# Performance work log

Hardware: AMD Instinct MI355X
Metric: run time of the kernel (lower is better)

The kernel has to match this reference:

```python
import jax, jax.numpy as jnp
import numpy as np
from jax import lax

DN = ('NCHW', 'OIHW', 'NCHW')


def conv3x3(x, w, groups=1):
    return lax.conv_general_dilated(x, w, window_strides=(1, 1),
                                    padding=((1, 1), (1, 1)),
                                    dimension_numbers=DN,
                                    feature_group_count=groups)


def conv1x1(x, w):
    return lax.conv_general_dilated(x, w, window_strides=(1, 1),
                                    padding=((0, 0), (0, 0)),
                                    dimension_numbers=DN)


def l2_normalize(t, eps=1e-12):
    n = jnp.sqrt(jnp.sum(t * t, axis=-1, keepdims=True))
    return t / jnp.maximum(n, eps)


def setup_inputs() -> dict:
    key = jax.random.key(0)
    ks = jax.random.split(key, 10)
    B, C, H, W = 4, 64, 256, 256
    heads = 8
    s = 0.05
    return {
        'x': jax.random.normal(ks[0], (B, C, H, W), jnp.float32),
        'w_iem': jax.random.normal(ks[1], (C, C, 3, 3), jnp.float32) * s,
        'w_nem': jax.random.normal(ks[2], (C, C, 3, 3), jnp.float32) * s,
        'w_iem_dw': jax.random.normal(ks[3], (C, 1, 3, 3), jnp.float32) * s,
        'w_nem_dw': jax.random.normal(ks[4], (C, 1, 3, 3), jnp.float32) * s,
        'w_q': jax.random.normal(ks[5], (C, C, 1, 1), jnp.float32) * s,
        'w_k': jax.random.normal(ks[6], (C, C, 1, 1), jnp.float32) * s,
        'w_v': jax.random.normal(ks[7], (C, C, 1, 1), jnp.float32) * s,
        'w_proj': jax.random.normal(ks[8], (C, C, 1, 1), jnp.float32) * s,
        'temperature': jnp.ones((1, heads, 1, 1, 1, 1), jnp.float32),
    }


def igam_forward(x, w_iem, w_nem, w_iem_dw, w_nem_dw, w_q, w_k, w_v, w_proj,
                 temperature, num_heads=8, window_size=8):
    b, c, h, w = x.shape
    ws = window_size
    pad_h = (ws - h % ws) % ws
    pad_w = (ws - w % ws) % ws
    if pad_h or pad_w:  # replicate pad on right/bottom (static)
        x = jnp.pad(x, ((0, 0), (0, 0), (0, pad_h), (0, pad_w)), mode='edge')
    hp, wp = x.shape[-2:]
    heads = num_heads
    d = c // heads
    nh, nw = hp // ws, wp // ws

    illumination_map = conv3x3(jax.nn.sigmoid(conv3x3(x, w_iem)), w_iem_dw, groups=c)
    noise_map = conv3x3(jax.nn.sigmoid(conv3x3(x, w_nem)), w_nem_dw, groups=c)
    illum_scalar = jnp.mean(illumination_map, axis=1, keepdims=True)  # (b,1,hp,wp)
    noise_scalar = jnp.mean(noise_map, axis=1, keepdims=True)

    q = conv1x1(illumination_map, w_q)
    k = conv1x1(noise_map, w_k)
    v = conv1x1(x, w_v)

    def to_windows(t):  # (b,c,hp,wp) -> (b,heads,nh,nw,ws*ws,d)
        t = t.reshape(b, heads, d, hp, wp).transpose(0, 1, 3, 4, 2)
        t = t.reshape(b, heads, nh, ws, nw, ws, d).transpose(0, 1, 2, 4, 3, 5, 6)
        return t.reshape(b, heads, nh, nw, ws * ws, d)

    def scalar_to_windows(t):  # (b,1,hp,wp) -> (b,1,nh,nw,ws*ws,1)
        t = t.reshape(b, 1, nh, ws, nw, ws).transpose(0, 1, 2, 4, 3, 5)
        return t.reshape(b, 1, nh, nw, ws * ws, 1)

    qw = l2_normalize(to_windows(q)) * (1.0 + scalar_to_windows(illum_scalar))
    kw = l2_normalize(to_windows(k)) * jnp.clip(1.0 - scalar_to_windows(noise_scalar), 0.0, 1.0)
    vw = to_windows(v)

    scale = d ** (-0.5)
    attn = jnp.einsum('bhnmqd,bhnmkd->bhnmqk', qw, kw) * scale * temperature
    attn = jax.nn.softmax(attn, axis=-1)
    outw = jnp.einsum('bhnmqk,bhnmkd->bhnmqd', attn, vw)

    # merge windows back to (b, c, hp, wp)
    outw = outw.reshape(b, heads, nh, nw, ws, ws, d).transpose(0, 1, 6, 2, 4, 3, 5)
    out = outw.reshape(b, heads * d, nh * ws, nw * ws)
    if pad_h or pad_w:
        out = out[:, :, :h, :w]
    return conv1x1(out, w_proj)


def reference(x, w_iem, w_nem, w_iem_dw, w_nem_dw, w_q, w_k, w_v, w_proj,
              temperature):
    return igam_forward(x, w_iem, w_nem, w_iem_dw, w_nem_dw, w_q, w_k, w_v,
                        w_proj, temperature)
```

## Files before the change

### kernel.cpp

```cpp
#include <hip/hip_runtime.h>
#include <math.h>

#define W_ 256
#define H_ 256
#define HW 65536
#define CC 64

typedef _Float16 h16;
typedef _Float16 half8 __attribute__((ext_vector_type(8)));
typedef float f32x4  __attribute__((ext_vector_type(4)));
typedef float f32x16 __attribute__((ext_vector_type(16)));

__device__ __forceinline__ unsigned pk2(float a, float b) {
  union { h16 h[2]; unsigned u; } c;
  c.h[0] = (h16)a; c.h[1] = (h16)b;
  return c.u;
}
__device__ __forceinline__ void plswap(unsigned &a, unsigned &b) {
  asm volatile("v_permlane32_swap_b32 %0, %1" : "+v"(a), "+v"(b));
}

__global__ __launch_bounds__(256) void k_wprep(
    const float* __restrict__ wi, const float* __restrict__ wn, h16* __restrict__ Bt)
{
  int i = blockIdx.x * 256 + threadIdx.x;
  if (i >= 128 * 576) return;
  int co = i / 576, k = i - co * 576;
  int tap = k >> 6, ci = k & 63;
  const float* src = (co < 64) ? wi : wn;
  int c = co & 63;
  Bt[i] = (h16)src[(c * 64 + ci) * 9 + tap];
}

__global__ __launch_bounds__(256) void k_wprep2(
    const float* __restrict__ wq, const float* __restrict__ wk,
    const float* __restrict__ wv, const float* __restrict__ wp,
    const float* __restrict__ wdw1, const float* __restrict__ wdw2,
    h16* __restrict__ W)
{
  int i = blockIdx.x * 256 + threadIdx.x;
  if (i >= 17536) return;
  if (i < 16384) {
    int m = i >> 12, e = i & 4095;
    const float* s = (m == 0) ? wq : (m == 1) ? wk : (m == 2) ? wv : wp;
    W[i] = (h16)s[e];
  } else {
    int e = i - 16384;
    int pass = e / 576, rem = e - pass * 576;
    int tap = rem >> 6, c = rem & 63;
    const float* s = pass ? wdw2 : wdw1;
    W[i] = (h16)s[c * 9 + tap];
  }
}

__global__ __launch_bounds__(256) void k_xpose(
    const float* __restrict__ x, h16* __restrict__ xT)
{
  __shared__ __align__(16) char sm[64 * 132];
  const int tid = threadIdx.x;
  const int xt = blockIdx.x, y = blockIdx.y, b = blockIdx.z;
  const int x0 = xt * 64;
  const float* xb = x + ((size_t)b * CC) * HW + y * W_ + x0;
  const int ci = tid >> 2, q = tid & 3;
#pragma unroll
  for (int k = 0; k < 4; ++k) {
    const int pc = q + k * 4;
    float4 v = *(const float4*)(xb + (size_t)ci * HW + pc * 4);
    const int px = pc * 4;
    *(h16*)(sm + (px + 0) * 132 + ci * 2) = (h16)v.x;
    *(h16*)(sm + (px + 1) * 132 + ci * 2) = (h16)v.y;
    *(h16*)(sm + (px + 2) * 132 + ci * 2) = (h16)v.z;
    *(h16*)(sm + (px + 3) * 132 + ci * 2) = (h16)v.w;
  }
  __syncthreads();
  h16* dst = xT + (((size_t)b * 256 + y) * 256 + x0) * 64;
#pragma unroll
  for (int it = 0; it < 2; ++it) {
    int task = tid + it * 256;
    int px = task >> 3, c8 = task & 7;
    int4 d = *(const int4*)(sm + px * 132 + c8 * 16);
    *(int4*)(dst + px * 64 + c8 * 8) = d;
  }
}

__global__ __launch_bounds__(512) void k_conv3x3x2(
    const h16* __restrict__ xT, const h16* __restrict__ Bt,
    h16* __restrict__ T1, h16* __restrict__ T2)
{
  __shared__ __align__(16) char lds[38016];

  const int tid = threadIdx.x;
  const int b = blockIdx.z, ry = blockIdx.y, cx = blockIdx.x;
  const int y0 = ry * 2, x0 = cx * 64;

  {
    const h16* xb = xT + ((size_t)b * 256) * 256 * 64;
    int4 zero4; zero4.x = zero4.y = zero4.z = zero4.w = 0;
#pragma unroll
    for (int it = 0; it < 5; ++it) {
      int idx = tid + it * 512;
      if (idx < 2112) {
        int pxr = idx >> 3, c8 = idx & 7;
        int r = pxr / 66, c = pxr - r * 66;
        int gy = y0 - 1 + r, gx = x0 - 1 + c;
        int4 d = zero4;
        if ((unsigned)gy < 256u && (unsigned)gx < 256u)
          d = *(const int4*)(xb + ((size_t)(gy * 256 + gx)) * 64 + c8 * 8);
        *(int4*)(lds + pxr * 144 + c8 * 16) = d;
      }
    }
  }
  __syncthreads();

  const int wv = tid >> 6, lane = tid & 63;
  const int wn_ = wv & 3;
  const int wm_ = wv >> 2;
  const int cob = wn_ * 32;
  const int pxb = wm_ * 64;
  const int lg = lane >> 4, lr = lane & 15;

  const char* pB[4];
#pragma unroll
  for (int pi = 0; pi < 4; ++pi) {
    int opx = (pxb + pi * 16 + lr) & 63;
    pB[pi] = lds + (wm_ * 66 + opx) * 144 + lg * 16;
  }
  const h16* wb0 = Bt + (size_t)(cob + lr) * 576 + lg * 8;
  const h16* wb1 = wb0 + 16 * 576;

  f32x4 acc[2][4];
#pragma unroll
  for (int i = 0; i < 2; ++i)
#pragma unroll
    for (int j = 0; j < 4; ++j) acc[i][j] = (f32x4){0.f, 0.f, 0.f, 0.f};

#pragma unroll
  for (int tap = 0; tap < 9; ++tap) {
    const int dy = tap / 3, dx = tap - dy * 3;
#pragma unroll
    for (int kh = 0; kh < 2; ++kh) {
      const int loff = (dy * 66 + dx) * 144 + kh * 64;
      const int koff = tap * 64 + kh * 32;
      half8 a0 = *(const half8*)(wb0 + koff);
      half8 a1 = *(const half8*)(wb1 + koff);
      half8 b0 = *(const half8*)(pB[0] + loff);
      half8 b1 = *(const half8*)(pB[1] + loff);
      half8 b2 = *(const half8*)(pB[2] + loff);
      half8 b3 = *(const half8*)(pB[3] + loff);
      acc[0][0] = __builtin_amdgcn_mfma_f32_16x16x32_f16(a0, b0, acc[0][0], 0, 0, 0);
      acc[0][1] = __builtin_amdgcn_mfma_f32_16x16x32_f16(a0, b1, acc[0][1], 0, 0, 0);
      acc[0][2] = __builtin_amdgcn_mfma_f32_16x16x32_f16(a0, b2, acc[0][2], 0, 0, 0);
      acc[0][3] = __builtin_amdgcn_mfma_f32_16x16x32_f16(a0, b3, acc[0][3], 0, 0, 0);
      acc[1][0] = __builtin_amdgcn_mfma_f32_16x16x32_f16(a1, b0, acc[1][0], 0, 0, 0);
      acc[1][1] = __builtin_amdgcn_mfma_f32_16x16x32_f16(a1, b1, acc[1][1], 0, 0, 0);
      acc[1][2] = __builtin_amdgcn_mfma_f32_16x16x32_f16(a1, b2, acc[1][2], 0, 0, 0);
      acc[1][3] = __builtin_amdgcn_mfma_f32_16x16x32_f16(a1, b3, acc[1][3], 0, 0, 0);
    }
  }
  __syncthreads();

#pragma unroll
  for (int ni = 0; ni < 2; ++ni) {
#pragma unroll
    for (int pi = 0; pi < 4; ++pi) {
      const int opx = (pxb + pi * 16 + lr) & 63;
      const int pxid = wm_ * 64 + opx;
      const int co = cob + ni * 16 + lg * 4;
      float s0 = 1.f / (1.f + __expf(-acc[ni][pi][0]));
      float s1 = 1.f / (1.f + __expf(-acc[ni][pi][1]));
      float s2 = 1.f / (1.f + __expf(-acc[ni][pi][2]));
      float s3 = 1.f / (1.f + __expf(-acc[ni][pi][3]));
      uint2 d; d.x = pk2(s0, s1); d.y = pk2(s2, s3);
      *(uint2*)(lds + pxid * 272 + co * 2) = d;
    }
  }
  __syncthreads();

  {
    int px = tid >> 3, chg = tid & 7;
#pragma unroll
    for (int seg = 0; seg < 4; ++seg) {
      int t = seg >> 1, rr = seg & 1;
      int4 d = *(const int4*)(lds + (rr * 64 + px) * 272 + t * 128 + chg * 16);
      h16* dst = (t ? T2 : T1) + (((size_t)b * 256 + (y0 + rr)) * 256 + (x0 + px)) * 64 + chg * 8;
      *(int4*)dst = d;
    }
  }
}

#define HALO 0
#define INC  0
#define DWW  14400
#define SIN  16704
#define INA  17216
#define INB  26432

__global__ __launch_bounds__(512, 8) void k_megaattn(
    const h16* __restrict__ T1g, const h16* __restrict__ T2g,
    const h16* __restrict__ xT, const h16* __restrict__ Wall,
    const float* __restrict__ temp, float* __restrict__ out)
{
  __shared__ __align__(16) char sm[35648];
  const int tid = threadIdx.x;
  const int wv = tid >> 6, lane = tid & 63;
  const int lg = lane >> 4, lr = lane & 15;
  const int wn = wv & 3;
  const int wm = wv >> 2;

  const int u = blockIdx.x;
  const int xcd = u & 7, idx = u >> 3;
  const int flat = xcd * 512 + idx;
  const int b = flat >> 10, rem = flat & 1023;
  const int wy = rem >> 5, wx = rem & 31;
  const int y0 = wy * 8, x0 = wx * 8;

  half8 wf[4][2];
#pragma unroll
  for (int m = 0; m < 4; ++m)
#pragma unroll
    for (int ks = 0; ks < 2; ++ks)
      wf[m][ks] = *(const half8*)(Wall + m * 4096 + (wn * 16 + lr) * 64 + ks * 32 + lg * 8);
  const float thv = temp[wn * 2 + (lg >> 1)];

  int4 zero4; zero4.x = zero4.y = zero4.z = zero4.w = 0;
  int4 h1r[2], h2r[2], xtr;
#pragma unroll
  for (int i = 0; i < 2; ++i) {
    int cc = tid + i * 512;
    bool act = cc < 800;
    int prow = act ? (cc >> 3) : 0;
    int c8 = cc & 7;
    int hy = prow / 10, hx = prow - hy * 10;
    int gy = y0 - 1 + hy, gx = x0 - 1 + hx;
    bool ok = act && (unsigned)gy < 256u && (unsigned)gx < 256u;
    size_t ga = (((size_t)b * 256 + gy) * 256 + gx) * (size_t)64 + c8 * 8;
    h1r[i] = ok ? *(const int4*)(T1g + ga) : zero4;
    h2r[i] = ok ? *(const int4*)(T2g + ga) : zero4;
  }
  const size_t wbase = (((size_t)b * 256 + y0) * 256 + x0) * 64;
  xtr = *(const int4*)(xT + wbase + (size_t)(tid >> 6) * 16384 + (tid & 63) * 8);

#pragma unroll
  for (int i = 0; i < 2; ++i) {
    int cc = tid + i * 512;
    if (cc < 800) *(int4*)(sm + HALO + (cc >> 3) * 144 + (cc & 7) * 16) = h1r[i];
  }
  if (tid < 144) {
    int4 d = *(const int4*)(Wall + 16384 + tid * 8);
    *(int4*)(sm + DWW + tid * 16) = d;
  }
  __syncthreads();

  const half8 hz8 = {(h16)0, (h16)0, (h16)0, (h16)0, (h16)0, (h16)0, (h16)0, (h16)0};
#pragma unroll
  for (int pass = 0; pass < 2; ++pass) {
    const int outb = pass ? INB : INA;
    {
      const int px = tid >> 3, c8 = tid & 7;
      const int py = px >> 3, pxx = px & 7;
      half8 af = hz8;
#pragma unroll
      for (int tap = 0; tap < 9; ++tap) {
        const int dy = tap / 3, dx = tap - dy * 3;
        half8 v  = *(const half8*)(sm + HALO + ((py + dy) * 10 + pxx + dx) * 144 + c8 * 16);
        half8 w8 = *(const half8*)(sm + DWW + pass * 1152 + tap * 128 + c8 * 16);
        af += v * w8;
      }
      *(half8*)(sm + outb + px * 144 + c8 * 16) = af;
    }
    __syncthreads();
    if (pass == 0) {
#pragma unroll
      for (int i = 0; i < 2; ++i) {
        int cc = tid + i * 512;
        if (cc < 800) *(int4*)(sm + HALO + (cc >> 3) * 144 + (cc & 7) * 16) = h2r[i];
      }
      __syncthreads();
    }
  }

  {
    int py = tid >> 6, off = tid & 63;
    int px = py * 8 + (off >> 3);
    *(int4*)(sm + INC + px * 144 + (off & 7) * 16) = xtr;
  }
  if (tid < 128) {
    int which = tid >> 6, px = tid & 63;
    const char* row = sm + (which ? INB : INA) + px * 144;
    float s = 0.f;
#pragma unroll
    for (int j = 0; j < 8; ++j) {
      half8 v = *(const half8*)(row + j * 16);
#pragma unroll
      for (int e = 0; e < 8; ++e) s += (float)v[e];
    }
    *(float*)(sm + SIN + which * 256 + px * 4) = s * (1.f / 64.f);
  }
  __syncthreads();

  f32x4 aq[2], ak[2], av[2];
#pragma unroll
  for (int pi = 0; pi < 2; ++pi) {
    aq[pi] = (f32x4){0.f, 0.f, 0.f, 0.f};
    ak[pi] = (f32x4){0.f, 0.f, 0.f, 0.f};
    av[pi] = (f32x4){0.f, 0.f, 0.f, 0.f};
  }
#pragma unroll
  for (int pi = 0; pi < 2; ++pi)
#pragma unroll
    for (int ks = 0; ks < 2; ++ks) {
      const int boff = (wm * 32 + pi * 16 + lr) * 144 + ks * 64 + lg * 16;
      half8 b0 = *(const half8*)(sm + INA + boff);
      half8 b1 = *(const half8*)(sm + INB + boff);
      half8 b2 = *(const half8*)(sm + INC + boff);
      aq[pi] = __builtin_amdgcn_mfma_f32_16x16x32_f16(wf[0][ks], b0, aq[pi], 0, 0, 0);
      ak[pi] = __builtin_amdgcn_mfma_f32_16x16x32_f16(wf[1][ks], b1, ak[pi], 0, 0, 0);
      av[pi] = __builtin_amdgcn_mfma_f32_16x16x32_f16(wf[2][ks], b2, av[pi], 0, 0, 0);
    }
  __syncthreads();

#pragma unroll
  for (int pi = 0; pi < 2; ++pi) {
    const int px = wm * 32 + pi * 16 + lr;
    const float si = *(const float*)(sm + SIN + px * 4);
    const float sn = *(const float*)(sm + SIN + 256 + px * 4);
    float s2 = aq[pi][0]*aq[pi][0] + aq[pi][1]*aq[pi][1] + aq[pi][2]*aq[pi][2] + aq[pi][3]*aq[pi][3];
    float qs = (1.f + si) * 0.35355339059327373f * thv /
               fmaxf(sqrtf(s2 + __shfl_xor(s2, 16)), 1e-12f);
    float k2 = ak[pi][0]*ak[pi][0] + ak[pi][1]*ak[pi][1] + ak[pi][2]*ak[pi][2] + ak[pi][3]*ak[pi][3];
    float ks2 = fminf(fmaxf(1.f - sn, 0.f), 1.f) /
                fmaxf(sqrtf(k2 + __shfl_xor(k2, 16)), 1e-12f);
    uint2 dq; dq.x = pk2(aq[pi][0]*qs, aq[pi][1]*qs); dq.y = pk2(aq[pi][2]*qs, aq[pi][3]*qs);
    uint2 dk; dk.x = pk2(ak[pi][0]*ks2, ak[pi][1]*ks2); dk.y = pk2(ak[pi][2]*ks2, ak[pi][3]*ks2);
    *(uint2*)(sm + INA + px * 144 + (wn * 16 + lg * 4) * 2) = dq;
    *(uint2*)(sm + INB + px * 144 + (wn * 16 + lg * 4) * 2) = dk;
#pragma unroll
    for (int r = 0; r < 4; ++r)
      *(h16*)(sm + INC + (wn * 16 + lg * 4 + r) * 144 + px * 2) = (h16)av[pi][r];
  }
  __syncthreads();

  const int l31 = lane & 31, hi = lane >> 5;
  const half8 hz = hz8;
  const f32x16 z16 = {0.f,0.f,0.f,0.f,0.f,0.f,0.f,0.f,0.f,0.f,0.f,0.f,0.f,0.f,0.f,0.f};
  {
    const int h = wv;
    half8 kfr[2], qfr[2];
#pragma unroll
    for (int kt = 0; kt < 2; ++kt)
      kfr[kt] = hi ? hz : *(const half8*)(sm + INB + (kt * 32 + l31) * 144 + h * 16);
#pragma unroll
    for (int qt = 0; qt < 2; ++qt)
      qfr[qt] = hi ? hz : *(const half8*)(sm + INA + (qt * 32 + l31) * 144 + h * 16);

#pragma unroll
    for (int qt = 0; qt < 2; ++qt) {
      f32x16 s0 = __builtin_amdgcn_mfma_f32_32x32x16_f16(kfr[0], qfr[qt], z16, 0, 0, 0);
      f32x16 s1 = __builtin_amdgcn_mfma_f32_32x32x16_f16(kfr[1], qfr[qt], z16, 0, 0, 0);
      float mx = s0[0];
#pragma unroll
      for (int i = 1; i < 16; ++i) mx = fmaxf(mx, s0[i]);
#pragma unroll
      for (int i = 0; i < 16; ++i) mx = fmaxf(mx, s1[i]);
      mx = fmaxf(mx, __shfl_xor(mx, 32));
      float sum = 0.f;
#pragma unroll
      for (int i = 0; i < 16; ++i) { s0[i] = __expf(s0[i] - mx); sum += s0[i]; }
#pragma unroll
      for (int i = 0; i < 16; ++i) { s1[i] = __expf(s1[i] - mx); sum += s1[i]; }
      sum += __shfl_xor(sum, 32);
      const float inv = 1.f / sum;
#pragma unroll
      for (int i = 0; i < 16; ++i) { s0[i] *= inv; s1[i] *= inv; }

      half8 pa[4];
#pragma unroll
      for (int st = 0; st < 4; ++st) {
        const int rb = (st & 1) * 8;
        float p0, p1, p2, p3, p4, p5, p6, p7;
        if (st < 2) {
          p0 = s0[rb+0]; p1 = s0[rb+1]; p2 = s0[rb+2]; p3 = s0[rb+3];
          p4 = s0[rb+4]; p5 = s0[rb+5]; p6 = s0[rb+6]; p7 = s0[rb+7];
        } else {
          p0 = s1[rb+0]; p1 = s1[rb+1]; p2 = s1[rb+2]; p3 = s1[rb+3];
          p4 = s1[rb+4]; p5 = s1[rb+5]; p6 = s1[rb+6]; p7 = s1[rb+7];
        }
        unsigned x0_ = pk2(p0, p1), x1_ = pk2(p2, p3);
        unsigned y0_ = pk2(p4, p5), y1_ = pk2(p6, p7);
        plswap(x0_, y0_);
        plswap(x1_, y1_);
        union { unsigned uu4[4]; half8 h; } uu;
        uu.uu4[0] = x0_; uu.uu4[1] = x1_; uu.uu4[2] = y0_; uu.uu4[3] = y1_;
        pa[st] = uu.h;
      }
      f32x16 oacc = z16;
#pragma unroll
      for (int st = 0; st < 4; ++st) {
        half8 vfr = (l31 < 8)
          ? *(const half8*)(sm + INC + (h * 8 + l31) * 144 + (st * 16 + hi * 8) * 2)
          : hz;
        oacc = __builtin_amdgcn_mfma_f32_32x32x16_f16(pa[st], vfr, oacc, 0, 0, 0);
      }
      if (l31 < 8) {
#pragma unroll
        for (int r = 0; r < 16; ++r) {
          const int q = qt * 32 + (r & 3) + 8 * (r >> 2) + 4 * hi;
          *(h16*)(sm + INA + q * 144 + (h * 8 + l31) * 2) = (h16)oacc[r];
        }
      }
    }
  }
  __syncthreads();

  f32x4 pacc[2];
#pragma unroll
  for (int pi = 0; pi < 2; ++pi) pacc[pi] = (f32x4){0.f, 0.f, 0.f, 0.f};
#pragma unroll
  for (int pi = 0; pi < 2; ++pi)
#pragma unroll
    for (int ks = 0; ks < 2; ++ks) {
      half8 bfr = *(const half8*)(sm + INA + (wm * 32 + pi * 16 + lr) * 144 + ks * 64 + lg * 16);
      pacc[pi] = __builtin_amdgcn_mfma_f32_16x16x32_f16(wf[3][ks], bfr, pacc[pi], 0, 0, 0);
    }
#pragma unroll
  for (int pi = 0; pi < 2; ++pi) {
    const int px = wm * 32 + pi * 16 + lr;
    const int py = px >> 3, pxx = px & 7;
    const int co = wn * 16 + lg * 4;
    float* ob = out + ((size_t)(b * CC + co)) * HW + (size_t)(y0 + py) * W_ + (x0 + pxx);
    ob[0]      = pacc[pi][0];
    ob[HW]     = pacc[pi][1];
    ob[2 * HW] = pacc[pi][2];
    ob[3 * HW] = pacc[pi][3];
  }
}

extern "C" void kernel_launch(void* const* d_in, const int* in_sizes, int n_in,
                              void* d_out, int out_size, void* d_ws, size_t ws_size,
                              hipStream_t stream) {
  const float* x        = (const float*)d_in[0];
  const float* w_iem    = (const float*)d_in[1];
  const float* w_nem    = (const float*)d_in[2];
  const float* w_iem_dw = (const float*)d_in[3];
  const float* w_nem_dw = (const float*)d_in[4];
  const float* w_q      = (const float*)d_in[5];
  const float* w_k      = (const float*)d_in[6];
  const float* w_v      = (const float*)d_in[7];
  const float* w_proj   = (const float*)d_in[8];
  const float* temp     = (const float*)d_in[9];
  float* outp = (float*)d_out;

  const size_t PLE = (size_t)4 * CC * HW;
  h16* h0   = (h16*)d_ws;
  h16* T1   = h0;
  h16* T2   = h0 + PLE;
  h16* xT   = h0 + 2 * PLE;
  h16* Bt   = h0 + 3 * PLE;
  h16* Wall = Bt + 73728;

  dim3 b256(256), b512(512);

  k_wprep    <<<dim3(288),        b256, 0, stream>>>(w_iem, w_nem, Bt);
  k_wprep2   <<<dim3(69),         b256, 0, stream>>>(w_q, w_k, w_v, w_proj,
                                                     w_iem_dw, w_nem_dw, Wall);
  k_xpose    <<<dim3(4, 256, 4),  b256, 0, stream>>>(x, xT);
  k_conv3x3x2<<<dim3(4, 128, 4),  b512, 0, stream>>>(xT, Bt, T1, T2);
  k_megaattn <<<dim3(4096),       b512, 0, stream>>>(T1, T2, xT, Wall, temp, outp);
}
```

Baseline: 210.7 us.

## Process two adjacent windows per block in attention megakernel with prefetched loads

Measured after the change: 393.7 us. 1.87x slower.

```diff
diff --git a/kernel.cpp b/kernel.cpp
--- a/kernel.cpp
+++ b/kernel.cpp
@@ -209,10 +209,11 @@
 
   const int u = blockIdx.x;
   const int xcd = u & 7, idx = u >> 3;
-  const int flat = xcd * 512 + idx;
-  const int b = flat >> 10, rem = flat & 1023;
-  const int wy = rem >> 5, wx = rem & 31;
-  const int y0 = wy * 8, x0 = wx * 8;
+  const int flat = xcd * 256 + idx;
+  const int fl0 = flat * 2;
+  const int b = fl0 >> 10, rem = fl0 & 1023;
+  const int wy = rem >> 5, wx0 = rem & 31;
+  const int y0 = wy * 8;
 
   half8 wf[4][2];
 #pragma unroll
@@ -223,27 +224,31 @@
   const float thv = temp[wn * 2 + (lg >> 1)];
 
   int4 zero4; zero4.x = zero4.y = zero4.z = zero4.w = 0;
-  int4 h1r[2], h2r[2], xtr;
+  int4 h1r[2][2], h2r[2][2], xtrv[2];
+#pragma unroll
+  for (int w2 = 0; w2 < 2; ++w2) {
+    const int x0w = (wx0 + w2) * 8;
+#pragma unroll
+    for (int i = 0; i < 2; ++i) {
+      int cc = tid + i * 512;
+      bool act = cc < 800;
+      int prow = act ? (cc >> 3) : 0;
+      int c8 = cc & 7;
+      int hy = prow / 10, hx = prow - hy * 10;
+      int gy = y0 - 1 + hy, gx = x0w - 1 + hx;
+      bool ok = act && (unsigned)gy < 256u && (unsigned)gx < 256u;
+      size_t ga = (((size_t)b * 256 + gy) * 256 + gx) * (size_t)64 + c8 * 8;
+      h1r[w2][i] = ok ? *(const int4*)(T1g + ga) : zero4;
+      h2r[w2][i] = ok ? *(const int4*)(T2g + ga) : zero4;
+    }
+    const size_t wbase = (((size_t)b * 256 + y0) * 256 + x0w) * 64;
+    xtrv[w2] = *(const int4*)(xT + wbase + (size_t)(tid >> 6) * 16384 + (tid & 63) * 8);
+  }
+
 #pragma unroll
   for (int i = 0; i < 2; ++i) {
     int cc = tid + i * 512;
-    bool act = cc < 800;
-    int prow = act ? (cc >> 3) : 0;
-    int c8 = cc & 7;
-    int hy = prow / 10, hx = prow - hy * 10;
-    int gy = y0 - 1 + hy, gx = x0 - 1 + hx;
-    bool ok = act && (unsigned)gy < 256u && (unsigned)gx < 256u;
-    size_t ga = (((size_t)b * 256 + gy) * 256 + gx) * (size_t)64 + c8 * 8;
-    h1r[i] = ok ? *(const int4*)(T1g + ga) : zero4;
-    h2r[i] = ok ? *(const int4*)(T2g + ga) : zero4;
-  }
-  const size_t wbase = (((size_t)b * 256 + y0) * 256 + x0) * 64;
-  xtr = *(const int4*)(xT + wbase + (size_t)(tid >> 6) * 16384 + (tid & 63) * 8);
-
-#pragma unroll
-  for (int i = 0; i < 2; ++i) {
-    int cc = tid + i * 512;
-    if (cc < 800) *(int4*)(sm + HALO + (cc >> 3) * 144 + (cc & 7) * 16) = h1r[i];
+    if (cc < 800) *(int4*)(sm + HALO + (cc >> 3) * 144 + (cc & 7) * 16) = h1r[0][i];
   }
   if (tid < 144) {
     int4 d = *(const int4*)(Wall + 16384 + tid * 8);
@@ -252,186 +257,201 @@
   __syncthreads();
 
   const half8 hz8 = {(h16)0, (h16)0, (h16)0, (h16)0, (h16)0, (h16)0, (h16)0, (h16)0};
-#pragma unroll
-  for (int pass = 0; pass < 2; ++pass) {
-    const int outb = pass ? INB : INA;
+  const f32x16 z16 = {0.f,0.f,0.f,0.f,0.f,0.f,0.f,0.f,0.f,0.f,0.f,0.f,0.f,0.f,0.f,0.f};
+
+#pragma unroll
+  for (int w2 = 0; w2 < 2; ++w2) {
+    const int x0 = (wx0 + w2) * 8;
+
+#pragma unroll
+    for (int pass = 0; pass < 2; ++pass) {
+      const int outb = pass ? INB : INA;
+      {
+        const int px = tid >> 3, c8 = tid & 7;
+        const int py = px >> 3, pxx = px & 7;
+        half8 af = hz8;
+#pragma unroll
+        for (int tap = 0; tap < 9; ++tap) {
+          const int dy = tap / 3, dx = tap - dy * 3;
+          half8 v  = *(const half8*)(sm + HALO + ((py + dy) * 10 + pxx + dx) * 144 + c8 * 16);
+          half8 w8 = *(const half8*)(sm + DWW + pass * 1152 + tap * 128 + c8 * 16);
+          af += v * w8;
+        }
+        *(half8*)(sm + outb + px * 144 + c8 * 16) = af;
+      }
+      __syncthreads();
+      if (pass == 0) {
+#pragma unroll
+        for (int i = 0; i < 2; ++i) {
+          int cc = tid + i * 512;
+          if (cc < 800) *(int4*)(sm + HALO + (cc >> 3) * 144 + (cc & 7) * 16) = h2r[w2][i];
+        }
+        __syncthreads();
+      }
+    }
+
     {
-      const int px = tid >> 3, c8 = tid & 7;
-      const int py = px >> 3, pxx = px & 7;
-      half8 af = hz8;
-#pragma unroll
-      for (int tap = 0; tap < 9; ++tap) {
-        const int dy = tap / 3, dx = tap - dy * 3;
-        half8 v  = *(const half8*)(sm + HALO + ((py + dy) * 10 + pxx + dx) * 144 + c8 * 16);
-        half8 w8 = *(const half8*)(sm + DWW + pass * 1152 + tap * 128 + c8 * 16);
-        af += v * w8;
-      }
-      *(half8*)(sm + outb + px * 144 + c8 * 16) = af;
+      int py = tid >> 6, off = tid & 63;
+      int px = py * 8 + (off >> 3);
+      *(int4*)(sm + INC + px * 144 + (off & 7) * 16) = xtrv[w2];
+    }
+    if (tid < 128) {
+      int which = tid >> 6, px = tid & 63;
+      const char* row = sm + (which ? INB : INA) + px * 144;
+      float s = 0.f;
+#pragma unroll
+      for (int j = 0; j < 8; ++j) {
+        half8 v = *(const half8*)(row + j * 16);
+#pragma unroll
+        for (int e = 0; e < 8; ++e) s += (float)v[e];
+      }
+      *(float*)(sm + SIN + which * 256 + px * 4) = s * (1.f / 64.f);
     }
     __syncthreads();
-    if (pass == 0) {
+
+    f32x4 aq[2], ak[2], av[2];
+#pragma unroll
+    for (int pi = 0; pi < 2; ++pi) {
+      aq[pi] = (f32x4){0.f, 0.f, 0.f, 0.f};
+      ak[pi] = (f32x4){0.f, 0.f, 0.f, 0.f};
+      av[pi] = (f32x4){0.f, 0.f, 0.f, 0.f};
+    }
+#pragma unroll
+    for (int pi = 0; pi < 2; ++pi)
+#pragma unroll
+      for (int ks = 0; ks < 2; ++ks) {
+        const int boff = (wm * 32 + pi * 16 + lr) * 144 + ks * 64 + lg * 16;
+        half8 b0 = *(const half8*)(sm + INA + boff);
+        half8 b1 = *(const half8*)(sm + INB + boff);
+        half8 b2 = *(const half8*)(sm + INC + boff);
+        aq[pi] = __builtin_amdgcn_mfma_f32_16x16x32_f16(wf[0][ks], b0, aq[pi], 0, 0, 0);
+        ak[pi] = __builtin_amdgcn_mfma_f32_16x16x32_f16(wf[1][ks], b1, ak[pi], 0, 0, 0);
+        av[pi] = __builtin_amdgcn_mfma_f32_16x16x32_f16(wf[2][ks], b2, av[pi], 0, 0, 0);
+      }
+    __syncthreads();
+
+#pragma unroll
+    for (int pi = 0; pi < 2; ++pi) {
+      const int px = wm * 32 + pi * 16 + lr;
+      const float si = *(const float*)(sm + SIN + px * 4);
+      const float sn = *(const float*)(sm + SIN + 256 + px * 4);
+      float s2 = aq[pi][0]*aq[pi][0] + aq[pi][1]*aq[pi][1] + aq[pi][2]*aq[pi][2] + aq[pi][3]*aq[pi][3];
+      float qs = (1.f + si) * 0.35355339059327373f * thv /
+                 fmaxf(sqrtf(s2 + __shfl_xor(s2, 16)), 1e-12f);
+      float k2 = ak[pi][0]*ak[pi][0] + ak[pi][1]*ak[pi][1] + ak[pi][2]*ak[pi][2] + ak[pi][3]*ak[pi][3];
+      float ks2 = fminf(fmaxf(1.f - sn, 0.f), 1.f) /
+                  fmaxf(sqrtf(k2 + __shfl_xor(k2, 16)), 1e-12f);
+      uint2 dq; dq.x = pk2(aq[pi][0]*qs, aq[pi][1]*qs); dq.y = pk2(aq[pi][2]*qs, aq[pi][3]*qs);
+      uint2 dk; dk.x = pk2(ak[pi][0]*ks2, ak[pi][1]*ks2); dk.y = pk2(ak[pi][2]*ks2, ak[pi][3]*ks2);
+      *(uint2*)(sm + INA + px * 144 + (wn * 16 + lg * 4) * 2) = dq;
+      *(uint2*)(sm + INB + px * 144 + (wn * 16 + lg * 4) * 2) = dk;
+#pragma unroll
+      for (int r = 0; r < 4; ++r)
+        *(h16*)(sm + INC + (wn * 16 + lg * 4 + r) * 144 + px * 2) = (h16)av[pi][r];
+    }
+    __syncthreads();
+
+    const int l31 = lane & 31, hi = lane >> 5;
+    {
+      const int h = wv;
+      half8 kfr[2], qfr[2];
+#pragma unroll
+      for (int kt = 0; kt < 2; ++kt)
+        kfr[kt] = hi ? hz8 : *(const half8*)(sm + INB + (kt * 32 + l31) * 144 + h * 16);
+#pragma unroll
+      for (int qt = 0; qt < 2; ++qt)
+        qfr[qt] = hi ? hz8 : *(const half8*)(sm + INA + (qt * 32 + l31) * 144 + h * 16);
+
+#pragma unroll
+      for (int qt = 0; qt < 2; ++qt) {
+        f32x16 s0 = __builtin_amdgcn_mfma_f32_32x32x16_f16(kfr[0], qfr[qt], z16, 0, 0, 0);
+        f32x16 s1 = __builtin_amdgcn_mfma_f32_32x32x16_f16(kfr[1], qfr[qt], z16, 0, 0, 0);
+        float mx = s0[0];
+#pragma unroll
+        for (int i = 1; i < 16; ++i) mx = fmaxf(mx, s0[i]);
+#pragma unroll
+        for (int i = 0; i < 16; ++i) mx = fmaxf(mx, s1[i]);
+        mx = fmaxf(mx, __shfl_xor(mx, 32));
+        float sum = 0.f;
+#pragma unroll
+        for (int i = 0; i < 16; ++i) { s0[i] = __expf(s0[i] - mx); sum += s0[i]; }
+#pragma unroll
+        for (int i = 0; i < 16; ++i) { s1[i] = __expf(s1[i] - mx); sum += s1[i]; }
+        sum += __shfl_xor(sum, 32);
+        const float inv = 1.f / sum;
+#pragma unroll
+        for (int i = 0; i < 16; ++i) { s0[i] *= inv; s1[i] *= inv; }
+
+        half8 pa[4];
+#pragma unroll
+        for (int st = 0; st < 4; ++st) {
+          const int rb = (st & 1) * 8;
+          float p0, p1, p2, p3, p4, p5, p6, p7;
+          if (st < 2) {
+            p0 = s0[rb+0]; p1 = s0[rb+1]; p2 = s0[rb+2]; p3 = s0[rb+3];
+            p4 = s0[rb+4]; p5 = s0[rb+5]; p6 = s0[rb+6]; p7 = s0[rb+7];
+          } else {
+            p0 = s1[rb+0]; p1 = s1[rb+1]; p2 = s1[rb+2]; p3 = s1[rb+3];
+            p4 = s1[rb+4]; p5 = s1[rb+5]; p6 = s1[rb+6]; p7 = s1[rb+7];
+          }
+          unsigned x0_ = pk2(p0, p1), x1_ = pk2(p2, p3);
+          unsigned y0_ = pk2(p4, p5), y1_ = pk2(p6, p7);
+          plswap(x0_, y0_);
+          plswap(x1_, y1_);
+          union { unsigned uu4[4]; half8 h; } uu;
+          uu.uu4[0] = x0_; uu.uu4[1] = x1_; uu.uu4[2] = y0_; uu.uu4[3] = y1_;
+          pa[st] = uu.h;
+        }
+        f32x16 oacc = z16;
+#pragma unroll
+        for (int st = 0; st < 4; ++st) {
+          half8 vfr = (l31 < 8)
+            ? *(const half8*)(sm + INC + (h * 8 + l31) * 144 + (st * 16 + hi * 8) * 2)
+            : hz8;
+          oacc = __builtin_amdgcn_mfma_f32_32x32x16_f16(pa[st], vfr, oacc, 0, 0, 0);
+        }
+        if (l31 < 8) {
+#pragma unroll
+          for (int r = 0; r < 16; ++r) {
+            const int q = qt * 32 + (r & 3) + 8 * (r >> 2) + 4 * hi;
+            *(h16*)(sm + INA + q * 144 + (h * 8 + l31) * 2) = (h16)oacc[r];
+          }
+        }
+      }
+    }
+    __syncthreads();
+
+    if (w2 == 0) {
 #pragma unroll
       for (int i = 0; i < 2; ++i) {
         int cc = tid + i * 512;
-        if (cc < 800) *(int4*)(sm + HALO + (cc >> 3) * 144 + (cc & 7) * 16) = h2r[i];
-      }
-      __syncthreads();
-    }
-  }
-
-  {
-    int py = tid >> 6, off = tid & 63;
-    int px = py * 8 + (off >> 3);
-    *(int4*)(sm + INC + px * 144 + (off & 7) * 16) = xtr;
-  }
-  if (tid < 128) {
-    int which = tid >> 6, px = tid & 63;
-    const char* row = sm + (which ? INB : INA) + px * 144;
-    float s = 0.f;
-#pragma unroll
-    for (int j = 0; j < 8; ++j) {
-      half8 v = *(const half8*)(row + j * 16);
-#pragma unroll
-      for (int e = 0; e < 8; ++e) s += (float)v[e];
-    }
-    *(float*)(sm + SIN + which * 256 + px * 4) = s * (1.f / 64.f);
-  }
-  __syncthreads();
-
-  f32x4 aq[2], ak[2], av[2];
-#pragma unroll
-  for (int pi = 0; pi < 2; ++pi) {
-    aq[pi] = (f32x4){0.f, 0.f, 0.f, 0.f};
-    ak[pi] = (f32x4){0.f, 0.f, 0.f, 0.f};
-    av[pi] = (f32x4){0.f, 0.f, 0.f, 0.f};
-  }
-#pragma unroll
-  for (int pi = 0; pi < 2; ++pi)
-#pragma unroll
-    for (int ks = 0; ks < 2; ++ks) {
-      const int boff = (wm * 32 + pi * 16 + lr) * 144 + ks * 64 + lg * 16;
-      half8 b0 = *(const half8*)(sm + INA + boff);
-      half8 b1 = *(const half8*)(sm + INB + boff);
-      half8 b2 = *(const half8*)(sm + INC + boff);
-      aq[pi] = __builtin_amdgcn_mfma_f32_16x16x32_f16(wf[0][ks], b0, aq[pi], 0, 0, 0);
-      ak[pi] = __builtin_amdgcn_mfma_f32_16x16x32_f16(wf[1][ks], b1, ak[pi], 0, 0, 0);
-      av[pi] = __builtin_amdgcn_mfma_f32_16x16x32_f16(wf[2][ks], b2, av[pi], 0, 0, 0);
-    }
-  __syncthreads();
-
-#pragma unroll
-  for (int pi = 0; pi < 2; ++pi) {
-    const int px = wm * 32 + pi * 16 + lr;
-    const float si = *(const float*)(sm + SIN + px * 4);
-    const float sn = *(const float*)(sm + SIN + 256 + px * 4);
-    float s2 = aq[pi][0]*aq[pi][0] + aq[pi][1]*aq[pi][1] + aq[pi][2]*aq[pi][2] + aq[pi][3]*aq[pi][3];
-    float qs = (1.f + si) * 0.35355339059327373f * thv /
-               fmaxf(sqrtf(s2 + __shfl_xor(s2, 16)), 1e-12f);
-    float k2 = ak[pi][0]*ak[pi][0] + ak[pi][1]*ak[pi][1] + ak[pi][2]*ak[pi][2] + ak[pi][3]*ak[pi][3];
-    float ks2 = fminf(fmaxf(1.f - sn, 0.f), 1.f) /
-                fmaxf(sqrtf(k2 + __shfl_xor(k2, 16)), 1e-12f);
-    uint2 dq; dq.x = pk2(aq[pi][0]*qs, aq[pi][1]*qs); dq.y = pk2(aq[pi][2]*qs, aq[pi][3]*qs);
-    uint2 dk; dk.x = pk2(ak[pi][0]*ks2, ak[pi][1]*ks2); dk.y = pk2(ak[pi][2]*ks2, ak[pi][3]*ks2);
-    *(uint2*)(sm + INA + px * 144 + (wn * 16 + lg * 4) * 2) = dq;
-    *(uint2*)(sm + INB + px * 144 + (wn * 16 + lg * 4) * 2) = dk;
-#pragma unroll
-    for (int r = 0; r < 4; ++r)
-      *(h16*)(sm + INC + (wn * 16 + lg * 4 + r) * 144 + px * 2) = (h16)av[pi][r];
-  }
-  __syncthreads();
-
-  const int l31 = lane & 31, hi = lane >> 5;
-  const half8 hz = hz8;
-  const f32x16 z16 = {0.f,0.f,0.f,0.f,0.f,0.f,0.f,0.f,0.f,0.f,0.f,0.f,0.f,0.f,0.f,0.f};
-  {
-    const int h = wv;
-    half8 kfr[2], qfr[2];
-#pragma unroll
-    for (int kt = 0; kt < 2; ++kt)
-      kfr[kt] = hi ? hz : *(const half8*)(sm + INB + (kt * 32 + l31) * 144 + h * 16);
-#pragma unroll
-    for (int qt = 0; qt < 2; ++qt)
-      qfr[qt] = hi ? hz : *(const half8*)(sm + INA + (qt * 32 + l31) * 144 + h * 16);
-
-#pragma unroll
-    for (int qt = 0; qt < 2; ++qt) {
-      f32x16 s0 = __builtin_amdgcn_mfma_f32_32x32x16_f16(kfr[0], qfr[qt], z16, 0, 0, 0);
-      f32x16 s1 = __builtin_amdgcn_mfma_f32_32x32x16_f16(kfr[1], qfr[qt], z16, 0, 0, 0);
-      float mx = s0[0];
-#pragma unroll
-      for (int i = 1; i < 16; ++i) mx = fmaxf(mx, s0[i]);
-#pragma unroll
-      for (int i = 0; i < 16; ++i) mx = fmaxf(mx, s1[i]);
-      mx = fmaxf(mx, __shfl_xor(mx, 32));
-      float sum = 0.f;
-#pragma unroll
-      for (int i = 0; i < 16; ++i) { s0[i] = __expf(s0[i] - mx); sum += s0[i]; }
-#pragma unroll
-      for (int i = 0; i < 16; ++i) { s1[i] = __expf(s1[i] - mx); sum += s1[i]; }
-      sum += __shfl_xor(sum, 32);
-      const float inv = 1.f / sum;
-#pragma unroll
-      for (int i = 0; i < 16; ++i) { s0[i] *= inv; s1[i] *= inv; }
-
-      half8 pa[4];
-#pragma unroll
-      for (int st = 0; st < 4; ++st) {
-        const int rb = (st & 1) * 8;
-        float p0, p1, p2, p3, p4, p5, p6, p7;
-        if (st < 2) {
-          p0 = s0[rb+0]; p1 = s0[rb+1]; p2 = s0[rb+2]; p3 = s0[rb+3];
-          p4 = s0[rb+4]; p5 = s0[rb+5]; p6 = s0[rb+6]; p7 = s0[rb+7];
-        } else {
-          p0 = s1[rb+0]; p1 = s1[rb+1]; p2 = s1[rb+2]; p3 = s1[rb+3];
-          p4 = s1[rb+4]; p5 = s1[rb+5]; p6 = s1[rb+6]; p7 = s1[rb+7];
-        }
-        unsigned x0_ = pk2(p0, p1), x1_ = pk2(p2, p3);
-        unsigned y0_ = pk2(p4, p5), y1_ = pk2(p6, p7);
-        plswap(x0_, y0_);
-        plswap(x1_, y1_);
-        union { unsigned uu4[4]; half8 h; } uu;
-        uu.uu4[0] = x0_; uu.uu4[1] = x1_; uu.uu4[2] = y0_; uu.uu4[3] = y1_;
-        pa[st] = uu.h;
-      }
-      f32x16 oacc = z16;
-#pragma unroll
-      for (int st = 0; st < 4; ++st) {
-        half8 vfr = (l31 < 8)
-          ? *(const half8*)(sm + INC + (h * 8 + l31) * 144 + (st * 16 + hi * 8) * 2)
-          : hz;
-        oacc = __builtin_amdgcn_mfma_f32_32x32x16_f16(pa[st], vfr, oacc, 0, 0, 0);
-      }
-      if (l31 < 8) {
-#pragma unroll
-        for (int r = 0; r < 16; ++r) {
-          const int q = qt * 32 + (r & 3) + 8 * (r >> 2) + 4 * hi;
-          *(h16*)(sm + INA + q * 144 + (h * 8 + l31) * 2) = (h16)oacc[r];
-        }
-      }
-    }
-  }
-  __syncthreads();
-
-  f32x4 pacc[2];
-#pragma unroll
-  for (int pi = 0; pi < 2; ++pi) pacc[pi] = (f32x4){0.f, 0.f, 0.f, 0.f};
-#pragma unroll
-  for (int pi = 0; pi < 2; ++pi)
-#pragma unroll
-    for (int ks = 0; ks < 2; ++ks) {
-      half8 bfr = *(const half8*)(sm + INA + (wm * 32 + pi * 16 + lr) * 144 + ks * 64 + lg * 16);
-      pacc[pi] = __builtin_amdgcn_mfma_f32_16x16x32_f16(wf[3][ks], bfr, pacc[pi], 0, 0, 0);
-    }
-#pragma unroll
-  for (int pi = 0; pi < 2; ++pi) {
-    const int px = wm * 32 + pi * 16 + lr;
-    const int py = px >> 3, pxx = px & 7;
-    const int co = wn * 16 + lg * 4;
-    float* ob = out + ((size_t)(b * CC + co)) * HW + (size_t)(y0 + py) * W_ + (x0 + pxx);
-    ob[0]      = pacc[pi][0];
-    ob[HW]     = pacc[pi][1];
-    ob[2 * HW] = pacc[pi][2];
-    ob[3 * HW] = pacc[pi][3];
+        if (cc < 800) *(int4*)(sm + HALO + (cc >> 3) * 144 + (cc & 7) * 16) = h1r[1][i];
+      }
+    }
+
+    f32x4 pacc[2];
+#pragma unroll
+    for (int pi = 0; pi < 2; ++pi) pacc[pi] = (f32x4){0.f, 0.f, 0.f, 0.f};
+#pragma unroll
+    for (int pi = 0; pi < 2; ++pi)
+#pragma unroll
+      for (int ks = 0; ks < 2; ++ks) {
+        half8 bfr = *(const half8*)(sm + INA + (wm * 32 + pi * 16 + lr) * 144 + ks * 64 + lg * 16);
+        pacc[pi] = __builtin_amdgcn_mfma_f32_16x16x32_f16(wf[3][ks], bfr, pacc[pi], 0, 0, 0);
+      }
+#pragma unroll
+    for (int pi = 0; pi < 2; ++pi) {
+      const int px = wm * 32 + pi * 16 + lr;
+      const int py = px >> 3, pxx = px & 7;
+      const int co = wn * 16 + lg * 4;
+      float* ob = out + ((size_t)(b * CC + co)) * HW + (size_t)(y0 + py) * W_ + (x0 + pxx);
+      ob[0]      = pacc[pi][0];
+      ob[HW]     = pacc[pi][1];
+      ob[2 * HW] = pacc[pi][2];
+      ob[3 * HW] = pacc[pi][3];
+    }
+
+    if (w2 == 0) __syncthreads();
   }
 }
 
@@ -465,5 +485,5 @@
                                                      w_iem_dw, w_nem_dw, Wall);
   k_xpose    <<<dim3(4, 256, 4),  b256, 0, stream>>>(x, xT);
   k_conv3x3x2<<<dim3(4, 128, 4),  b512, 0, stream>>>(xT, Bt, T1, T2);
-  k_megaattn <<<dim3(4096),       b512, 0, stream>>>(T1, T2, xT, Wall, temp, outp);
-}
+  k_megaattn <<<dim3(2048),       b512, 0, stream>>>(T1, T2, xT, Wall, temp, outp);
+}
```
